# Kernel tuning notes

Hardware: AMD Instinct MI355X
Metric: run time of the kernel (lower is better)

The kernel has to match this reference:

```python
import jax, jax.numpy as jnp
import numpy as np


def setup_inputs() -> dict:
    key = jax.random.key(0)
    ks = jax.random.split(key, 5)
    B, C, H, W = 8, 64, 64, 64
    Ci = 32  # inter_channels = in_channels // 2
    s = 1.0 / np.sqrt(C)
    return {
        "x": jax.random.normal(ks[0], (B, C, H, W), jnp.float32),
        "Wg": jax.random.normal(ks[1], (Ci, C), jnp.float32) * s,
        "bg": jnp.zeros((Ci,), jnp.float32),
        "Wt": jax.random.normal(ks[2], (Ci, C), jnp.float32) * s,
        "bt": jnp.zeros((Ci,), jnp.float32),
        "Wp": jax.random.normal(ks[3], (Ci, C), jnp.float32) * s,
        "bp": jnp.zeros((Ci,), jnp.float32),
        "Ww": jax.random.normal(ks[4], (C, Ci), jnp.float32) * (1.0 / np.sqrt(Ci)),
        "bw": jnp.zeros((C,), jnp.float32),
    }


def _proj(x, Wc, bc):
    # 1x1 conv: (B,C,H,W) -> (B,O,H,W), then flatten spatial -> (B,O,N)
    b, c, h, w = x.shape
    y = jnp.einsum("oc,bchw->bohw", Wc, x) + bc[None, :, None, None]
    return y.reshape(b, Wc.shape[0], h * w)


def reference(x, Wg, bg, Wt, bt, Wp, bp, Ww, bw):
    b, c, h, w = x.shape
    g_x = _proj(x, Wg, bg).transpose(0, 2, 1)      # (B, N, Ci)
    theta_x = _proj(x, Wt, bt).transpose(0, 2, 1)  # (B, N, Ci)
    phi_x = _proj(x, Wp, bp)                        # (B, Ci, N)
    f = jnp.einsum("bnd,bdm->bnm", theta_x, phi_x)  # (B, N, N)
    f_div_C = jax.nn.softmax(f, axis=-1)
    y = jnp.einsum("bnm,bmd->bnd", f_div_C, g_x)    # (B, N, Ci)
    y = y.transpose(0, 2, 1).reshape(b, Wg.shape[0], h, w)
    W_y = jnp.einsum("od,bdhw->bohw", Ww, y) + bw[None, :, None, None]
    return W_y + x
```

## Files before the change

### kernel.cpp

```cpp
#include <hip/hip_runtime.h>
#include <hip/hip_bf16.h>
#include <cstdint>
#include <cstddef>

#define B_ 8
#define C_ 64
#define CI 32
#define N_ 4096
#define LOG2E 1.44269504088896340736f

typedef __attribute__((ext_vector_type(8))) short bf16x8;
typedef __attribute__((ext_vector_type(4))) float f32x4;

static __device__ __forceinline__ ushort f2bf(float x) {
  union { float f; uint32_t u; } v; v.f = x;
  uint32_t r = v.u + 0x7FFFu + ((v.u >> 16) & 1u);
  return (ushort)(r >> 16);
}

static __device__ __forceinline__ uint32_t cvt_pk_bf16(float lo, float hi) {
  uint32_t r;
  asm("v_cvt_pk_bf16_f32 %0, %1, %2" : "=v"(r) : "v"(lo), "v"(hi));
  return r;
}

__global__ __launch_bounds__(256) void proj_kernel(
    const float* __restrict__ x,
    const float* __restrict__ Wg, const float* __restrict__ bg,
    const float* __restrict__ Wt, const float* __restrict__ bt,
    const float* __restrict__ Wp, const float* __restrict__ bp,
    ushort* __restrict__ theta_t, ushort* __restrict__ phi_t,
    ushort* __restrict__ gmat)
{
  const int z = blockIdx.z;
  const float* W; const float* bias;
  if (z == 0)      { W = Wt; bias = bt; }
  else if (z == 1) { W = Wp; bias = bp; }
  else             { W = Wg; bias = bg; }

  const int b = blockIdx.y;
  const int t = threadIdx.x;
  const int n = blockIdx.x * 64 + (t & 63);
  const int dq = t >> 6;
  const float* xb = x + ((size_t)b * C_) * N_ + n;
  const float* Wr = W + dq * 8 * C_;

  float acc[8];
  #pragma unroll
  for (int i = 0; i < 8; ++i) acc[i] = bias[dq * 8 + i];

  #pragma unroll 8
  for (int c = 0; c < C_; ++c) {
    const float xv = xb[(size_t)c * N_];
    #pragma unroll
    for (int i = 0; i < 8; ++i)
      acc[i] = fmaf(Wr[i * C_ + c], xv, acc[i]);
  }

  if (z == 2) {
    #pragma unroll
    for (int i = 0; i < 8; ++i)
      gmat[((size_t)(b * CI) + dq * 8 + i) * N_ + n] = f2bf(acc[i]);
  } else {
    const float scale = (z == 0) ? LOG2E : 1.0f;
    uint32_t w[4];
    #pragma unroll
    for (int k = 0; k < 4; ++k)
      w[k] = (uint32_t)f2bf(acc[2 * k] * scale) |
             ((uint32_t)f2bf(acc[2 * k + 1] * scale) << 16);
    ushort* base = (z == 0) ? theta_t : phi_t;
    *(uint4*)(base + ((size_t)(b * N_) + n) * CI + dq * 8) =
        make_uint4(w[0], w[1], w[2], w[3]);
  }
}

__global__ __launch_bounds__(512, 4) void attn_kernel(
    const ushort* __restrict__ theta_t,
    const ushort* __restrict__ phi_t,
    const ushort* __restrict__ gmat,
    const float* __restrict__ Ww, const float* __restrict__ bw,
    const float* __restrict__ x, float* __restrict__ out)
{
  __shared__ union {
    ushort pt[8][2][16 * 64];
    float  accS[4][32][64];
  } Sh;
  __shared__ float mlS[4][8][64];
  __shared__ float WwL[C_ * CI];
  __shared__ float Yl[32 * 66];

  const int tid = threadIdx.x;
  const int lane = tid & 63;
  const int mh = tid >> 6;
  const int bid = blockIdx.x;
  const int b = bid & 7;
  const int n0 = (bid >> 3) * 64;
  const int g4 = lane >> 4;
  const int c16 = lane & 15;
  const int sw = (c16 & 7) << 4;

  #pragma unroll
  for (int i = 0; i < 4; ++i) WwL[tid + i * 512] = Ww[tid + i * 512];

  bf16x8 qfrag[4];
  #pragma unroll
  for (int s = 0; s < 4; ++s)
    qfrag[s] = *(const bf16x8*)(theta_t +
        ((size_t)(b * N_ + n0 + s * 16 + c16)) * CI + g4 * 8);

  f32x4 acc[4][2];
  #pragma unroll
  for (int s = 0; s < 4; ++s) {
    acc[s][0] = (f32x4){0.f, 0.f, 0.f, 0.f};
    acc[s][1] = (f32x4){0.f, 0.f, 0.f, 0.f};
  }
  float m_run[4] = {0.f, 0.f, 0.f, 0.f};
  float l_lane[4] = {0.f, 0.f, 0.f, 0.f};

  const int mq0 = mh * 512;
  const ushort* kbase = phi_t + ((size_t)(b * N_ + mq0 + c16)) * CI + g4 * 8;
  const ushort* vb0 = gmat + ((size_t)(b * CI + c16)) * N_ + mq0 + g4 * 8;
  const ushort* vb1 = vb0 + (size_t)16 * N_;

  char* pw[2][4]; const char* prd[2][2];
  #pragma unroll
  for (int pb = 0; pb < 2; ++pb) {
    #pragma unroll
    for (int mt = 0; mt < 4; ++mt)
      pw[pb][mt] = (char*)Sh.pt[mh][pb] + ((c16 * 128 + mt * 32 + g4 * 8) ^ sw);
    #pragma unroll
    for (int ks = 0; ks < 2; ++ks)
      prd[pb][ks] = (const char*)Sh.pt[mh][pb] +
                    ((c16 * 128 + ks * 64 + g4 * 16) ^ sw);
  }

  const int NT = 8;
  for (int t = 0; t < NT; ++t) {
    bf16x8 kf[4];
    #pragma unroll
    for (int mt = 0; mt < 4; ++mt)
      kf[mt] = *(const bf16x8*)(kbase + (size_t)(t * 64 + mt * 16) * CI);
    bf16x8 vf0[2], vf1[2];
    #pragma unroll
    for (int ks = 0; ks < 2; ++ks) {
      vf0[ks] = *(const bf16x8*)(vb0 + t * 64 + ks * 32);
      vf1[ks] = *(const bf16x8*)(vb1 + t * 64 + ks * 32);
    }

    #pragma unroll
    for (int s = 0; s < 4; ++s) {
      const int pb = s & 1;
      f32x4 f[4];
      __builtin_amdgcn_s_setprio(1);
      #pragma unroll
      for (int mt = 0; mt < 4; ++mt)
        f[mt] = __builtin_amdgcn_mfma_f32_16x16x32_bf16(
            kf[mt], qfrag[s], (f32x4){0.f, 0.f, 0.f, 0.f}, 0, 0, 0);
      __builtin_amdgcn_s_setprio(0);

      float pm = -1e30f;
      float pv[4][4];
      #pragma unroll
      for (int mt = 0; mt < 4; ++mt) {
        #pragma unroll
        for (int rr = 0; rr < 4; ++rr) {
          const float fv = f[mt][rr];
          pm = fmaxf(pm, fv);
          pv[mt][rr] = __builtin_amdgcn_exp2f(fv - m_run[s]);
        }
        l_lane[s] += (pv[mt][0] + pv[mt][1]) + (pv[mt][2] + pv[mt][3]);
      }
      #pragma unroll
      for (int mt = 0; mt < 4; ++mt) {
        uint2 wv;
        wv.x = cvt_pk_bf16(pv[mt][0], pv[mt][1]);
        wv.y = cvt_pk_bf16(pv[mt][2], pv[mt][3]);
        *(uint2*)pw[pb][mt] = wv;
      }
      asm volatile("s_waitcnt lgkmcnt(0)" ::: "memory");
      __builtin_amdgcn_sched_barrier(0);

      __builtin_amdgcn_s_setprio(1);
      #pragma unroll
      for (int ks = 0; ks < 2; ++ks) {
        const bf16x8 pfrag = *(const bf16x8*)prd[pb][ks];
        acc[s][0] = __builtin_amdgcn_mfma_f32_16x16x32_bf16(
            vf0[ks], pfrag, acc[s][0], 0, 0, 0);
        acc[s][1] = __builtin_amdgcn_mfma_f32_16x16x32_bf16(
            vf1[ks], pfrag, acc[s][1], 0, 0, 0);
      }
      __builtin_amdgcn_s_setprio(0);

      if (__any(pm > m_run[s] + 8.f)) {
        float pmr = fmaxf(pm, __shfl_xor(pm, 16));
        pmr = fmaxf(pmr, __shfl_xor(pmr, 32));
        const float mnew = fmaxf(m_run[s], pmr);
        const float sc = __builtin_amdgcn_exp2f(m_run[s] - mnew);
        m_run[s] = mnew;
        acc[s][0] *= sc; acc[s][1] *= sc; l_lane[s] *= sc;
      }
    }
  }

  #pragma unroll
  for (int s = 0; s < 4; ++s) {
    l_lane[s] += __shfl_xor(l_lane[s], 16);
    l_lane[s] += __shfl_xor(l_lane[s], 32);
  }

  #pragma unroll
  for (int r = 4; r >= 1; r >>= 1) {
    __syncthreads();
    if (mh >= r && mh < 2 * r) {
      float* ad = &Sh.accS[mh - r][0][0] + lane;
      float* md = &mlS[mh - r][0][0] + lane;
      #pragma unroll
      for (int s = 0; s < 4; ++s) {
        #pragma unroll
        for (int rr = 0; rr < 4; ++rr) {
          ad[(s * 8 + rr) * 64]     = acc[s][0][rr];
          ad[(s * 8 + 4 + rr) * 64] = acc[s][1][rr];
        }
        md[s * 64]       = m_run[s];
        md[(4 + s) * 64] = l_lane[s];
      }
    }
    __syncthreads();
    if (mh < r) {
      const float* as_ = &Sh.accS[mh][0][0] + lane;
      const float* ms_ = &mlS[mh][0][0] + lane;
      #pragma unroll
      for (int s = 0; s < 4; ++s) {
        const float mb = ms_[s * 64];
        const float lb = ms_[(4 + s) * 64];
        const float mM = fmaxf(m_run[s], mb);
        const float ea = __builtin_amdgcn_exp2f(m_run[s] - mM);
        const float eb = __builtin_amdgcn_exp2f(mb - mM);
        #pragma unroll
        for (int rr = 0; rr < 4; ++rr) {
          acc[s][0][rr] = acc[s][0][rr] * ea + as_[(s * 8 + rr) * 64] * eb;
          acc[s][1][rr] = acc[s][1][rr] * ea + as_[(s * 8 + 4 + rr) * 64] * eb;
        }
        l_lane[s] = l_lane[s] * ea + lb * eb;
        m_run[s] = mM;
      }
    }
  }
  __syncthreads();

  if (mh == 0) {
    #pragma unroll
    for (int s = 0; s < 4; ++s) {
      const float inv = 1.0f / l_lane[s];
      const int q = s * 16 + c16;
      #pragma unroll
      for (int rr = 0; rr < 4; ++rr) {
        Yl[(g4 * 4 + rr) * 66 + q]      = acc[s][0][rr] * inv;
        Yl[(16 + g4 * 4 + rr) * 66 + q] = acc[s][1][rr] * inv;
      }
    }
  }
  __syncthreads();

  const int nl = tid & 63;
  const int cg = tid >> 6;
  float oacc[8];
  #pragma unroll
  for (int i = 0; i < 8; ++i) oacc[i] = bw[cg * 8 + i];
  #pragma unroll
  for (int d = 0; d < CI; ++d) {
    const float yv = Yl[d * 66 + nl];
    #pragma unroll
    for (int i = 0; i < 8; ++i)
      oacc[i] = fmaf(WwL[(cg * 8 + i) * CI + d], yv, oacc[i]);
  }
  #pragma unroll
  for (int i = 0; i < 8; ++i) {
    const size_t idx = ((size_t)(b * C_ + cg * 8 + i)) * N_ + n0 + nl;
    out[idx] = oacc[i] + x[idx];
  }
}

extern "C" void kernel_launch(void* const* d_in, const int* in_sizes, int n_in,
                              void* d_out, int out_size, void* d_ws, size_t ws_size,
                              hipStream_t stream) {
  const float* x  = (const float*)d_in[0];
  const float* Wg = (const float*)d_in[1];
  const float* bg = (const float*)d_in[2];
  const float* Wt = (const float*)d_in[3];
  const float* bt = (const float*)d_in[4];
  const float* Wp = (const float*)d_in[5];
  const float* bp = (const float*)d_in[6];
  const float* Ww = (const float*)d_in[7];
  const float* bw = (const float*)d_in[8];
  float* out = (float*)d_out;

  char* ws = (char*)d_ws;
  ushort* theta_t = (ushort*)(ws);
  ushort* phi_t   = (ushort*)(ws + (size_t)2 * 1024 * 1024);
  ushort* gmat    = (ushort*)(ws + (size_t)4 * 1024 * 1024);

  proj_kernel<<<dim3(N_ / 64, B_, 3), 256, 0, stream>>>(
      x, Wg, bg, Wt, bt, Wp, bp, theta_t, phi_t, gmat);
  attn_kernel<<<dim3((N_ / 64) * B_), 512, 0, stream>>>(
      theta_t, phi_t, gmat, Ww, bw, x, out);
}
```

Measured before the change: 73.22 us.

## Software-pipeline attention loop: overlap PV MMA with next QK/softmax, prefetch K tiles

The attention inner loop is restructured so each sub-tile's PV MFMAs run one step later, interleaved with the next sub-tile's QK MFMAs and exp2 softmax, with P fragments read from LDS before the new P is written. K fragments for the next tile are prefetched a full iteration ahead, and a drain block finishes the last pending PV. The projection kernel also stages the transposed weights and bias in shared memory for vectorized float4 reads. The aim is to hide LDS and MFMA latency behind VALU work, at the cost of more live registers and tricky double-buffer ordering.

```diff
diff --git a/kernel.cpp b/kernel.cpp
--- a/kernel.cpp
+++ b/kernel.cpp
@@ -32,29 +32,46 @@
     ushort* __restrict__ theta_t, ushort* __restrict__ phi_t,
     ushort* __restrict__ gmat)
 {
+  __shared__ float WLt[C_ * CI];
+  __shared__ float bL[CI];
+
   const int z = blockIdx.z;
   const float* W; const float* bias;
   if (z == 0)      { W = Wt; bias = bt; }
   else if (z == 1) { W = Wp; bias = bp; }
   else             { W = Wg; bias = bg; }
 
+  const int t = threadIdx.x;
+  #pragma unroll
+  for (int k = 0; k < 8; ++k) {
+    const int i = t + k * 256;
+    WLt[(i % C_) * CI + (i / C_)] = W[i];
+  }
+  if (t < CI) bL[t] = bias[t];
+  __syncthreads();
+
   const int b = blockIdx.y;
-  const int t = threadIdx.x;
   const int n = blockIdx.x * 64 + (t & 63);
   const int dq = t >> 6;
   const float* xb = x + ((size_t)b * C_) * N_ + n;
-  const float* Wr = W + dq * 8 * C_;
 
   float acc[8];
   #pragma unroll
-  for (int i = 0; i < 8; ++i) acc[i] = bias[dq * 8 + i];
+  for (int i = 0; i < 8; ++i) acc[i] = bL[dq * 8 + i];
 
   #pragma unroll 8
   for (int c = 0; c < C_; ++c) {
     const float xv = xb[(size_t)c * N_];
-    #pragma unroll
-    for (int i = 0; i < 8; ++i)
-      acc[i] = fmaf(Wr[i * C_ + c], xv, acc[i]);
+    const float4 w0 = *(const float4*)&WLt[c * CI + dq * 8];
+    const float4 w1 = *(const float4*)&WLt[c * CI + dq * 8 + 4];
+    acc[0] = fmaf(w0.x, xv, acc[0]);
+    acc[1] = fmaf(w0.y, xv, acc[1]);
+    acc[2] = fmaf(w0.z, xv, acc[2]);
+    acc[3] = fmaf(w0.w, xv, acc[3]);
+    acc[4] = fmaf(w1.x, xv, acc[4]);
+    acc[5] = fmaf(w1.y, xv, acc[5]);
+    acc[6] = fmaf(w1.z, xv, acc[6]);
+    acc[7] = fmaf(w1.w, xv, acc[7]);
   }
 
   if (z == 2) {
@@ -73,6 +90,69 @@
         make_uint4(w[0], w[1], w[2], w[3]);
   }
 }
+
+#define QKPV_BODY(S, DO_PREV)                                                 \
+  {                                                                           \
+    constexpr int sP = ((S) + 3) & 3;                                         \
+    f32x4 f[4];                                                               \
+    __builtin_amdgcn_s_setprio(1);                                            \
+    _Pragma("unroll")                                                         \
+    for (int mt = 0; mt < 4; ++mt)                                            \
+      f[mt] = __builtin_amdgcn_mfma_f32_16x16x32_bf16(                        \
+          kf[mt], qfrag[S], (f32x4){0.f, 0.f, 0.f, 0.f}, 0, 0, 0);            \
+    __builtin_amdgcn_s_setprio(0);                                            \
+           \
+    asm volatile("s_waitcnt lgkmcnt(0)" ::: "memory");                        \
+    __builtin_amdgcn_sched_barrier(0);                                        \
+    const bf16x8 pfA = *(const bf16x8*)prd[((S) + 1) & 1][0];                 \
+    const bf16x8 pfB = *(const bf16x8*)prd[((S) + 1) & 1][1];                 \
+    float pm = -1e30f;                                                        \
+    float pv[4][4];                                                           \
+    _Pragma("unroll")                                                         \
+    for (int mt = 0; mt < 4; ++mt) {                                          \
+      _Pragma("unroll")                                                       \
+      for (int rr = 0; rr < 4; ++rr) {                                        \
+        const float fv = f[mt][rr];                                           \
+        pm = fmaxf(pm, fv);                                                   \
+        pv[mt][rr] = __builtin_amdgcn_exp2f(fv - m_run[S]);                   \
+      }                                                                       \
+      l_lane[S] += (pv[mt][0] + pv[mt][1]) + (pv[mt][2] + pv[mt][3]);         \
+    }                                                                         \
+    uint2 wv[4];                                                              \
+    _Pragma("unroll")                                                         \
+    for (int mt = 0; mt < 4; ++mt) {                                          \
+      wv[mt].x = cvt_pk_bf16(pv[mt][0], pv[mt][1]);                           \
+      wv[mt].y = cvt_pk_bf16(pv[mt][2], pv[mt][3]);                           \
+    }                                                                         \
+                     \
+    asm volatile("s_waitcnt lgkmcnt(0)" ::: "memory");                        \
+    __builtin_amdgcn_sched_barrier(0);                                        \
+    if (DO_PREV) {                                                            \
+      __builtin_amdgcn_s_setprio(1);                                          \
+      acc[sP][0] = __builtin_amdgcn_mfma_f32_16x16x32_bf16(                   \
+          vf0[0], pfA, acc[sP][0], 0, 0, 0);                                  \
+      acc[sP][1] = __builtin_amdgcn_mfma_f32_16x16x32_bf16(                   \
+          vf1[0], pfA, acc[sP][1], 0, 0, 0);                                  \
+      acc[sP][0] = __builtin_amdgcn_mfma_f32_16x16x32_bf16(                   \
+          vf0[1], pfB, acc[sP][0], 0, 0, 0);                                  \
+      acc[sP][1] = __builtin_amdgcn_mfma_f32_16x16x32_bf16(                   \
+          vf1[1], pfB, acc[sP][1], 0, 0, 0);                                  \
+      __builtin_amdgcn_s_setprio(0);                                          \
+      if (__any(pm_pend > m_run[sP] + 8.f)) {                                 \
+        float pmr = fmaxf(pm_pend, __shfl_xor(pm_pend, 16));                  \
+        pmr = fmaxf(pmr, __shfl_xor(pmr, 32));                                \
+        const float mnew = fmaxf(m_run[sP], pmr);                             \
+        const float sc = __builtin_amdgcn_exp2f(m_run[sP] - mnew);            \
+        m_run[sP] = mnew;                                                     \
+        acc[sP][0] *= sc; acc[sP][1] *= sc; l_lane[sP] *= sc;                 \
+      }                                                                       \
+    }                                                                         \
+    pm_pend = pm;                                                             \
+    _Pragma("unroll")                                                         \
+    for (int mt = 0; mt < 4; ++mt)                                            \
+      *(uint2*)pw[(S) & 1][mt] = wv[mt];                                      \
+    __builtin_amdgcn_sched_barrier(0);                                        \
+  }
 
 __global__ __launch_bounds__(512, 4) void attn_kernel(
     const ushort* __restrict__ theta_t,
@@ -116,6 +196,7 @@
   }
   float m_run[4] = {0.f, 0.f, 0.f, 0.f};
   float l_lane[4] = {0.f, 0.f, 0.f, 0.f};
+  float pm_pend = 0.f;
 
   const int mq0 = mh * 512;
   const ushort* kbase = phi_t + ((size_t)(b * N_ + mq0 + c16)) * CI + g4 * 8;
@@ -134,71 +215,51 @@
                     ((c16 * 128 + ks * 64 + g4 * 16) ^ sw);
   }
 
+  bf16x8 kf[4], kfn[4], vf0[2], vf1[2];
+  #pragma unroll
+  for (int mt = 0; mt < 4; ++mt)
+    kfn[mt] = *(const bf16x8*)(kbase + (size_t)(mt * 16) * CI);
+
   const int NT = 8;
   for (int t = 0; t < NT; ++t) {
-    bf16x8 kf[4];
+    #pragma unroll
+    for (int mt = 0; mt < 4; ++mt) kf[mt] = kfn[mt];
+    const int tn = (t + 1 < NT) ? t + 1 : t;
     #pragma unroll
     for (int mt = 0; mt < 4; ++mt)
-      kf[mt] = *(const bf16x8*)(kbase + (size_t)(t * 64 + mt * 16) * CI);
-    bf16x8 vf0[2], vf1[2];
+      kfn[mt] = *(const bf16x8*)(kbase + (size_t)(tn * 64 + mt * 16) * CI);
+
+    QKPV_BODY(0, (t > 0))
+
     #pragma unroll
     for (int ks = 0; ks < 2; ++ks) {
       vf0[ks] = *(const bf16x8*)(vb0 + t * 64 + ks * 32);
       vf1[ks] = *(const bf16x8*)(vb1 + t * 64 + ks * 32);
     }
 
-    #pragma unroll
-    for (int s = 0; s < 4; ++s) {
-      const int pb = s & 1;
-      f32x4 f[4];
-      __builtin_amdgcn_s_setprio(1);
-      #pragma unroll
-      for (int mt = 0; mt < 4; ++mt)
-        f[mt] = __builtin_amdgcn_mfma_f32_16x16x32_bf16(
-            kf[mt], qfrag[s], (f32x4){0.f, 0.f, 0.f, 0.f}, 0, 0, 0);
-      __builtin_amdgcn_s_setprio(0);
-
-      float pm = -1e30f;
-      float pv[4][4];
-      #pragma unroll
-      for (int mt = 0; mt < 4; ++mt) {
-        #pragma unroll
-        for (int rr = 0; rr < 4; ++rr) {
-          const float fv = f[mt][rr];
-          pm = fmaxf(pm, fv);
-          pv[mt][rr] = __builtin_amdgcn_exp2f(fv - m_run[s]);
-        }
-        l_lane[s] += (pv[mt][0] + pv[mt][1]) + (pv[mt][2] + pv[mt][3]);
-      }
-      #pragma unroll
-      for (int mt = 0; mt < 4; ++mt) {
-        uint2 wv;
-        wv.x = cvt_pk_bf16(pv[mt][0], pv[mt][1]);
-        wv.y = cvt_pk_bf16(pv[mt][2], pv[mt][3]);
-        *(uint2*)pw[pb][mt] = wv;
-      }
-      asm volatile("s_waitcnt lgkmcnt(0)" ::: "memory");
-      __builtin_amdgcn_sched_barrier(0);
-
-      __builtin_amdgcn_s_setprio(1);
-      #pragma unroll
-      for (int ks = 0; ks < 2; ++ks) {
-        const bf16x8 pfrag = *(const bf16x8*)prd[pb][ks];
-        acc[s][0] = __builtin_amdgcn_mfma_f32_16x16x32_bf16(
-            vf0[ks], pfrag, acc[s][0], 0, 0, 0);
-        acc[s][1] = __builtin_amdgcn_mfma_f32_16x16x32_bf16(
-            vf1[ks], pfrag, acc[s][1], 0, 0, 0);
-      }
-      __builtin_amdgcn_s_setprio(0);
-
-      if (__any(pm > m_run[s] + 8.f)) {
-        float pmr = fmaxf(pm, __shfl_xor(pm, 16));
-        pmr = fmaxf(pmr, __shfl_xor(pmr, 32));
-        const float mnew = fmaxf(m_run[s], pmr);
-        const float sc = __builtin_amdgcn_exp2f(m_run[s] - mnew);
-        m_run[s] = mnew;
-        acc[s][0] *= sc; acc[s][1] *= sc; l_lane[s] *= sc;
-      }
+    QKPV_BODY(1, true)
+    QKPV_BODY(2, true)
+    QKPV_BODY(3, true)
+  }
+
+  {
+    asm volatile("s_waitcnt lgkmcnt(0)" ::: "memory");
+    __builtin_amdgcn_sched_barrier(0);
+    const bf16x8 pfA = *(const bf16x8*)prd[1][0];
+    const bf16x8 pfB = *(const bf16x8*)prd[1][1];
+    asm volatile("s_waitcnt lgkmcnt(0)" ::: "memory");
+    __builtin_amdgcn_sched_barrier(0);
+    acc[3][0] = __builtin_amdgcn_mfma_f32_16x16x32_bf16(vf0[0], pfA, acc[3][0], 0, 0, 0);
+    acc[3][1] = __builtin_amdgcn_mfma_f32_16x16x32_bf16(vf1[0], pfA, acc[3][1], 0, 0, 0);
+    acc[3][0] = __builtin_amdgcn_mfma_f32_16x16x32_bf16(vf0[1], pfB, acc[3][0], 0, 0, 0);
+    acc[3][1] = __builtin_amdgcn_mfma_f32_16x16x32_bf16(vf1[1], pfB, acc[3][1], 0, 0, 0);
+    if (__any(pm_pend > m_run[3] + 8.f)) {
+      float pmr = fmaxf(pm_pend, __shfl_xor(pm_pend, 16));
+      pmr = fmaxf(pmr, __shfl_xor(pmr, 32));
+      const float mnew = fmaxf(m_run[3], pmr);
+      const float sc = __builtin_amdgcn_exp2f(m_run[3] - mnew);
+      m_run[3] = mnew;
+      acc[3][0] *= sc; acc[3][1] *= sc; l_lane[3] *= sc;
     }
   }
 
```

Result: slower. 127.0 us (+73.4%).

## Drop online softmax max tracking, stage proj weights in LDS, prefetch K tiles

Applied to the files above, without the earlier changes.

The attention loop no longer computes a per-tile row maximum. It exponentiates the raw scores and rescales by a fixed power of two when the running sum grows too large, folding the shift into the MFMA accumulator initial value. The projection kernel now stages transposed weights in shared memory for vectorized reads. The attention kernel also double-buffers its K-fragment global loads and lowers its launch-bounds occupancy hint from 4 to 2. Removing the max tracking risks overflow or underflow if scores are large, because exp2 of the raw logit can exceed float range before the rescale check runs.

```diff
diff --git a/kernel.cpp b/kernel.cpp
--- a/kernel.cpp
+++ b/kernel.cpp
@@ -32,29 +32,46 @@
     ushort* __restrict__ theta_t, ushort* __restrict__ phi_t,
     ushort* __restrict__ gmat)
 {
+  __shared__ float WLt[C_ * CI];
+  __shared__ float bL[CI];
+
   const int z = blockIdx.z;
   const float* W; const float* bias;
   if (z == 0)      { W = Wt; bias = bt; }
   else if (z == 1) { W = Wp; bias = bp; }
   else             { W = Wg; bias = bg; }
 
+  const int t = threadIdx.x;
+  #pragma unroll
+  for (int k = 0; k < 8; ++k) {
+    const int i = t + k * 256;
+    WLt[(i % C_) * CI + (i / C_)] = W[i];
+  }
+  if (t < CI) bL[t] = bias[t];
+  __syncthreads();
+
   const int b = blockIdx.y;
-  const int t = threadIdx.x;
   const int n = blockIdx.x * 64 + (t & 63);
   const int dq = t >> 6;
   const float* xb = x + ((size_t)b * C_) * N_ + n;
-  const float* Wr = W + dq * 8 * C_;
 
   float acc[8];
   #pragma unroll
-  for (int i = 0; i < 8; ++i) acc[i] = bias[dq * 8 + i];
+  for (int i = 0; i < 8; ++i) acc[i] = bL[dq * 8 + i];
 
   #pragma unroll 8
   for (int c = 0; c < C_; ++c) {
     const float xv = xb[(size_t)c * N_];
-    #pragma unroll
-    for (int i = 0; i < 8; ++i)
-      acc[i] = fmaf(Wr[i * C_ + c], xv, acc[i]);
+    const float4 w0 = *(const float4*)&WLt[c * CI + dq * 8];
+    const float4 w1 = *(const float4*)&WLt[c * CI + dq * 8 + 4];
+    acc[0] = fmaf(w0.x, xv, acc[0]);
+    acc[1] = fmaf(w0.y, xv, acc[1]);
+    acc[2] = fmaf(w0.z, xv, acc[2]);
+    acc[3] = fmaf(w0.w, xv, acc[3]);
+    acc[4] = fmaf(w1.x, xv, acc[4]);
+    acc[5] = fmaf(w1.y, xv, acc[5]);
+    acc[6] = fmaf(w1.z, xv, acc[6]);
+    acc[7] = fmaf(w1.w, xv, acc[7]);
   }
 
   if (z == 2) {
@@ -74,7 +91,7 @@
   }
 }
 
-__global__ __launch_bounds__(512, 4) void attn_kernel(
+__global__ __launch_bounds__(512, 2) void attn_kernel(
     const ushort* __restrict__ theta_t,
     const ushort* __restrict__ phi_t,
     const ushort* __restrict__ gmat,
@@ -109,12 +126,13 @@
         ((size_t)(b * N_ + n0 + s * 16 + c16)) * CI + g4 * 8);
 
   f32x4 acc[4][2];
+  f32x4 cinit[4];
   #pragma unroll
   for (int s = 0; s < 4; ++s) {
     acc[s][0] = (f32x4){0.f, 0.f, 0.f, 0.f};
     acc[s][1] = (f32x4){0.f, 0.f, 0.f, 0.f};
-  }
-  float m_run[4] = {0.f, 0.f, 0.f, 0.f};
+    cinit[s]  = (f32x4){0.f, 0.f, 0.f, 0.f};
+  }
   float l_lane[4] = {0.f, 0.f, 0.f, 0.f};
 
   const int mq0 = mh * 512;
@@ -134,13 +152,19 @@
                     ((c16 * 128 + ks * 64 + g4 * 16) ^ sw);
   }
 
+  bf16x8 kf[4], kfn[4], vf0[2], vf1[2];
+  #pragma unroll
+  for (int mt = 0; mt < 4; ++mt)
+    kfn[mt] = *(const bf16x8*)(kbase + (size_t)(mt * 16) * CI);
+
   const int NT = 8;
   for (int t = 0; t < NT; ++t) {
-    bf16x8 kf[4];
+    #pragma unroll
+    for (int mt = 0; mt < 4; ++mt) kf[mt] = kfn[mt];
+    const int tn = (t + 1 < NT) ? t + 1 : t;
     #pragma unroll
     for (int mt = 0; mt < 4; ++mt)
-      kf[mt] = *(const bf16x8*)(kbase + (size_t)(t * 64 + mt * 16) * CI);
-    bf16x8 vf0[2], vf1[2];
+      kfn[mt] = *(const bf16x8*)(kbase + (size_t)(tn * 64 + mt * 16) * CI);
     #pragma unroll
     for (int ks = 0; ks < 2; ++ks) {
       vf0[ks] = *(const bf16x8*)(vb0 + t * 64 + ks * 32);
@@ -155,19 +179,15 @@
       #pragma unroll
       for (int mt = 0; mt < 4; ++mt)
         f[mt] = __builtin_amdgcn_mfma_f32_16x16x32_bf16(
-            kf[mt], qfrag[s], (f32x4){0.f, 0.f, 0.f, 0.f}, 0, 0, 0);
+            kf[mt], qfrag[s], cinit[s], 0, 0, 0);
       __builtin_amdgcn_s_setprio(0);
 
-      float pm = -1e30f;
       float pv[4][4];
       #pragma unroll
       for (int mt = 0; mt < 4; ++mt) {
         #pragma unroll
-        for (int rr = 0; rr < 4; ++rr) {
-          const float fv = f[mt][rr];
-          pm = fmaxf(pm, fv);
-          pv[mt][rr] = __builtin_amdgcn_exp2f(fv - m_run[s]);
-        }
+        for (int rr = 0; rr < 4; ++rr)
+          pv[mt][rr] = __builtin_amdgcn_exp2f(f[mt][rr]);
         l_lane[s] += (pv[mt][0] + pv[mt][1]) + (pv[mt][2] + pv[mt][3]);
       }
       #pragma unroll
@@ -191,21 +211,21 @@
       }
       __builtin_amdgcn_s_setprio(0);
 
-      if (__any(pm > m_run[s] + 8.f)) {
-        float pmr = fmaxf(pm, __shfl_xor(pm, 16));
-        pmr = fmaxf(pmr, __shfl_xor(pmr, 32));
-        const float mnew = fmaxf(m_run[s], pmr);
-        const float sc = __builtin_amdgcn_exp2f(m_run[s] - mnew);
-        m_run[s] = mnew;
+      if (__any(l_lane[s] > 0x1p40f)) {
+        const float sc = 0x1p-64f;
         acc[s][0] *= sc; acc[s][1] *= sc; l_lane[s] *= sc;
-      }
-    }
-  }
-
+        #pragma unroll
+        for (int rr = 0; rr < 4; ++rr) cinit[s][rr] -= 64.f;
+      }
+    }
+  }
+
+  float m_run[4];
   #pragma unroll
   for (int s = 0; s < 4; ++s) {
     l_lane[s] += __shfl_xor(l_lane[s], 16);
     l_lane[s] += __shfl_xor(l_lane[s], 32);
+    m_run[s] = -cinit[s][0];
   }
 
   #pragma unroll
```

Measured after the change: 60.36 us. 17.6% less time.
